# Kernel optimization log

Hardware: AMD Instinct MI355X
Metric: run time of the kernel (lower is better)

Reference implementation:

```python
import jax, jax.numpy as jnp
import numpy as np

B, L, H = 2, 2048, 2048
NH, KVH = 16, 4
D = H // NH          # 128
G = NH // KVH        # 4 query heads per kv head
LN_EPS = 1e-12


def setup_inputs() -> dict:
    key = jax.random.key(0)
    ks = jax.random.split(key, 6)
    s = 0.02
    return {
        "hidden_state": jax.random.normal(ks[0], (B, L, H), jnp.float32),
        "mask": jnp.zeros((B, 1, 1, L), jnp.float32),
        "Wq": jax.random.normal(ks[1], (H, H), jnp.float32) * s,
        "bq": jnp.zeros((H,), jnp.float32),
        "Wk": jax.random.normal(ks[2], (KVH * D, H), jnp.float32) * s,
        "bk": jnp.zeros((KVH * D,), jnp.float32),
        "Wv": jax.random.normal(ks[3], (KVH * D, H), jnp.float32) * s,
        "bv": jnp.zeros((KVH * D,), jnp.float32),
        "Wo": jax.random.normal(ks[4], (H, H), jnp.float32) * s,
        "bo": jnp.zeros((H,), jnp.float32),
        "ln_g": jnp.ones((H,), jnp.float32),
        "ln_b": jnp.zeros((H,), jnp.float32),
    }


def _layernorm(x, g, b):
    mu = jnp.mean(x, axis=-1, keepdims=True)
    var = jnp.mean(jnp.square(x - mu), axis=-1, keepdims=True)
    return (x - mu) * jax.lax.rsqrt(var + LN_EPS) * g + b


def reference(hidden_state, mask, Wq, bq, Wk, bk, Wv, bv, Wo, bo, ln_g, ln_b):
    x = hidden_state
    # projections: b l (h d)
    q = x @ Wq.T + bq            # [B,L,NH*D]
    k = x @ Wk.T + bk            # [B,L,KVH*D]
    v = x @ Wv.T + bv            # [B,L,KVH*D]
    # b l (h d) -> b h l d, with q heads grouped per kv head (GQA broadcast,
    # mathematically identical to repeat_kv + dense SDPA)
    q = q.reshape(B, L, KVH, G, D).transpose(0, 2, 3, 1, 4)   # [B,KVH,G,L,D]
    k = k.reshape(B, L, KVH, D).transpose(0, 2, 1, 3)         # [B,KVH,L,D]
    v = v.reshape(B, L, KVH, D).transpose(0, 2, 1, 3)         # [B,KVH,L,D]
    scale = 1.0 / jnp.sqrt(jnp.float32(D))
    scores = jnp.einsum('bkgld,bkmd->bkglm', q, k) * scale    # [B,KVH,G,L,L]
    scores = scores + mask[:, :, None]                         # broadcast [B,1,1,1,L]
    attn = jax.nn.softmax(scores, axis=-1)
    out = jnp.einsum('bkglm,bkmd->bkgld', attn, v)            # [B,KVH,G,L,D]
    out = out.transpose(0, 3, 1, 2, 4).reshape(B, L, H)       # b h l d -> b l (h d)
    # SelfOutput: dense + residual + layernorm
    out = out @ Wo.T + bo
    return _layernorm(out + x, ln_g, ln_b)
```

## Files before the change

### kernel.cpp

```cpp
#include <hip/hip_runtime.h>
#include <math.h>

typedef short v8s __attribute__((ext_vector_type(8)));
typedef short v4s __attribute__((ext_vector_type(4)));
typedef float v4f __attribute__((ext_vector_type(4)));
typedef unsigned long long ull;

constexpr int L_ = 2048;
constexpr int H_ = 2048;
constexpr float LOG2E = 1.4426950408889634f;
constexpr float QSCALE = 0.08838834764831845f * LOG2E;

__device__ inline unsigned short f2bf(float f) {
    unsigned int u = __float_as_uint(f);
    u += 0x7fffu + ((u >> 16) & 1u);
    return (unsigned short)(u >> 16);
}

__device__ inline unsigned int pk2bf(float lo, float hi) {
    unsigned int a = __float_as_uint(lo) + 0x8000u;
    unsigned int b = __float_as_uint(hi) + 0x8000u;
    return __builtin_amdgcn_perm(b, a, 0x07060302);
}

__device__ inline void async16(const void* g, void* l) {
    __builtin_amdgcn_global_load_lds(
        (const __attribute__((address_space(1))) unsigned int*)g,
        (__attribute__((address_space(3))) unsigned int*)l, 16, 0, 0);
}

__global__ __launch_bounds__(256) void conv_all(
    const float* __restrict__ x,  const float* __restrict__ wq,
    const float* __restrict__ wk, const float* __restrict__ wv,
    const float* __restrict__ wo, const float* __restrict__ mask,
    unsigned short* __restrict__ xb, unsigned short* __restrict__ wqkvb,
    unsigned short* __restrict__ wob, float* __restrict__ maskL)
{
    int u = blockIdx.x * 256 + threadIdx.x;
    const float* s;
    unsigned short* d;
    if (u < 1048576)      { s = x  + (size_t)u * 8;             d = xb   + (size_t)u * 8; }
    else if (u < 1572864) { size_t t = (size_t)(u - 1048576) * 8; s = wq + t; d = wqkvb + t; }
    else if (u < 1703936) { size_t t = (size_t)(u - 1572864) * 8; s = wk + t; d = wqkvb + (size_t)2048 * 2048 + t; }
    else if (u < 1835008) { size_t t = (size_t)(u - 1703936) * 8; s = wv + t; d = wqkvb + (size_t)2560 * 2048 + t; }
    else if (u < 2359296) { size_t t = (size_t)(u - 1835008) * 8; s = wo + t; d = wob + t; }
    else if (u < 2359808) {
        int m = (u - 2359296) * 8;
        float4 a = *(const float4*)(mask + m);
        float4 b = *(const float4*)(mask + m + 4);
        float4 oa = {a.x * LOG2E, a.y * LOG2E, a.z * LOG2E, a.w * LOG2E};
        float4 ob = {b.x * LOG2E, b.y * LOG2E, b.z * LOG2E, b.w * LOG2E};
        *(float4*)(maskL + m) = oa;
        *(float4*)(maskL + m + 4) = ob;
        return;
    } else return;
    float4 a = *(const float4*)s;
    float4 b = *(const float4*)(s + 4);
    v8s o;
    o[0] = (short)f2bf(a.x); o[1] = (short)f2bf(a.y);
    o[2] = (short)f2bf(a.z); o[3] = (short)f2bf(a.w);
    o[4] = (short)f2bf(b.x); o[5] = (short)f2bf(b.y);
    o[6] = (short)f2bf(b.z); o[7] = (short)f2bf(b.w);
    *(v8s*)d = o;
}

template <int MODE>
__global__ __launch_bounds__(256) void gemm_mfma(
    const unsigned short* __restrict__ A, const unsigned short* __restrict__ W,
    const float* __restrict__ b0, const float* __restrict__ b1,
    const float* __restrict__ b2,
    unsigned short* __restrict__ oq, unsigned short* __restrict__ ok,
    unsigned short* __restrict__ ov,
    float* __restrict__ of, const float* __restrict__ resid,
    int K, int N)
{
    __shared__ short SM[3 * 8192];

    const int tid  = threadIdx.x;
    const int lane = tid & 63;
    const int wave = tid >> 6;
    const int lid  = lane & 15;
    const int g    = lane >> 4;
    const int wr   = wave >> 1, wc = wave & 1;
    const int row0 = blockIdx.y * 128, col0 = blockIdx.x * 128;

    auto stage = [&](int k0, int buf) {
#pragma unroll
        for (int i = 0; i < 2; ++i) {
            int idx = tid + i * 256;
            int r = idx >> 2, s = idx & 3;
            int c = s ^ ((r >> 1) & 3);
            async16(A + (size_t)(row0 + r) * K + k0 + c * 8,
                    &SM[buf * 8192 + idx * 8]);
            async16(W + (size_t)(col0 + r) * K + k0 + c * 8,
                    &SM[buf * 8192 + 4096 + idx * 8]);
        }
    };

    v4f acc[4][4];
#pragma unroll
    for (int i = 0; i < 4; ++i)
#pragma unroll
        for (int j = 0; j < 4; ++j) acc[i][j] = (v4f){0.f, 0.f, 0.f, 0.f};

    stage(0, 0);
    stage(32, 1);
    int p = 0;
    for (int k0 = 0; k0 < K; k0 += 32) {
        __syncthreads();
        if (k0 + 64 < K) {
            int nb = p + 2; if (nb >= 3) nb -= 3;
            stage(k0 + 64, nb);
        }
        const short* As = &SM[p * 8192];
        const short* Bs = &SM[p * 8192 + 4096];

        v8s af[4], bf[4];
#pragma unroll
        for (int t = 0; t < 4; ++t) {
            int ra = wr * 64 + t * 16 + lid;
            int rb = wc * 64 + t * 16 + lid;
            af[t] = *(const v8s*)&As[ra * 32 + ((g ^ ((ra >> 1) & 3)) * 8)];
            bf[t] = *(const v8s*)&Bs[rb * 32 + ((g ^ ((rb >> 1) & 3)) * 8)];
        }
#pragma unroll
        for (int mt = 0; mt < 4; ++mt)
#pragma unroll
            for (int nt = 0; nt < 4; ++nt)
                acc[mt][nt] = __builtin_amdgcn_mfma_f32_16x16x32_bf16(
                    af[mt], bf[nt], acc[mt][nt], 0, 0, 0);
        if (++p == 3) p = 0;
    }

    const int crow = row0 + wr * 64, ccol = col0 + wc * 64;
    if (MODE == 0) {
#pragma unroll
        for (int mt = 0; mt < 4; ++mt)
#pragma unroll
            for (int nt = 0; nt < 4; ++nt) {
                int cc = ccol + nt * 16 + lid;
                float bb = b0[cc];
#pragma unroll
                for (int r = 0; r < 4; ++r) {
                    int rr = crow + mt * 16 + g * 4 + r;
                    of[(size_t)rr * N + cc] =
                        acc[mt][nt][r] + bb + resid[(size_t)rr * N + cc];
                }
            }
    } else {
        const int seg = (col0 < 2048) ? 0 : (col0 < 2560 ? 1 : 2);
#pragma unroll
        for (int mt = 0; mt < 4; ++mt)
#pragma unroll
            for (int nt = 0; nt < 4; ++nt) {
                int cc = ccol + nt * 16 + lid;
                if (seg == 0) {
                    float bb = b0[cc];
#pragma unroll
                    for (int r = 0; r < 4; ++r) {
                        int rr = crow + mt * 16 + g * 4 + r;
                        oq[(size_t)rr * 2048 + cc] =
                            f2bf((acc[mt][nt][r] + bb) * QSCALE);
                    }
                } else if (seg == 1) {
                    float bb = b1[cc - 2048];
#pragma unroll
                    for (int r = 0; r < 4; ++r) {
                        int rr = crow + mt * 16 + g * 4 + r;
                        ok[(size_t)rr * 512 + (cc - 2048)] =
                            f2bf(acc[mt][nt][r] + bb);
                    }
                } else {
                    float bb = b2[cc - 2560];
#pragma unroll
                    for (int r = 0; r < 4; ++r) {
                        int rr = crow + mt * 16 + g * 4 + r;
                        ov[(size_t)rr * 512 + (cc - 2560)] =
                            f2bf(acc[mt][nt][r] + bb);
                    }
                }
            }
    }
}

__global__ __launch_bounds__(256) void transpose_v(
    const unsigned short* __restrict__ V, unsigned short* __restrict__ Vt)
{
    __shared__ unsigned short T[64][72];
    const int r0 = blockIdx.y * 64;
    const int c0 = blockIdx.x * 64;
    const int tid = threadIdx.x;
    const int r = tid >> 3, c8 = (tid & 7) * 8;
#pragma unroll
    for (int h = 0; h < 2; ++h) {
        v8s val = *(const v8s*)&V[(size_t)(r0 + h * 32 + r) * 512 + c0 + c8];
#pragma unroll
        for (int e = 0; e < 8; ++e) T[c8 + e][h * 32 + r] = (unsigned short)val[e];
    }
    __syncthreads();
#pragma unroll
    for (int h = 0; h < 2; ++h) {
        int idx = tid + h * 256;
        int ci = idx >> 3, ch = (idx & 7) * 8;
        int t32 = ch & 32;
        int gg  = (ch >> 3) & 3;
        int kb  = t32 + gg * 4;
        uint2 lo = *(const uint2*)&T[ci][kb];
        uint2 hi = *(const uint2*)&T[ci][kb + 16];
        union { uint4 u; v8s v; } o;
        o.u.x = lo.x; o.u.y = lo.y; o.u.z = hi.x; o.u.w = hi.y;
        int rr = r0 + ch;
        *(v8s*)&Vt[((size_t)((rr >> 11) * 512 + c0 + ci)) * 2048 + (rr & 2047)] = o.v;
    }
}

__global__ __launch_bounds__(256) void flash_mfma(
    const unsigned short* __restrict__ Q,
    const unsigned short* __restrict__ K,
    const unsigned short* __restrict__ Vt,
    const float* __restrict__ maskL,
    unsigned short* __restrict__ AO)
{
    __shared__ short K_s[2][32 * 128];
    __shared__ short V_s[2][128 * 32];

    const int tid  = threadIdx.x;
    const int lane = tid & 63;
    const int wave = tid >> 6;
    const int lid  = lane & 15;
    const int g    = lane >> 4;
    const int lh   = (lid >> 2) & 3;
    const int h    = blockIdx.y;
    const int b    = blockIdx.z;
    const int kvh  = h >> 2;
    const int q0   = blockIdx.x * 128;
    const int wq   = wave * 32;

    const unsigned short* pK;
    const unsigned short* pV;
    {
        int kr = tid >> 4, ks = tid & 15;
        pK = K + ((size_t)(b * L_ + kr)) * 512 + kvh * 128 +
             ((ks ^ (kr & 15)) * 8);
        int vd = tid >> 2, vs = tid & 3;
        pV = Vt + ((size_t)(b * 512 + kvh * 128 + vd)) * 2048 +
             ((vs ^ ((vd >> 2) & 3)) * 8);
    }

    v8s bq[2][4];
    {
        const size_t base = ((size_t)(b * L_ + q0 + wq + lid)) * 2048 + h * 128;
#pragma unroll
        for (int qt = 0; qt < 2; ++qt)
#pragma unroll
            for (int kc = 0; kc < 4; ++kc)
                bq[qt][kc] = *(const v8s*)(Q + base + (size_t)qt * 16 * 2048 +
                                           kc * 32 + g * 8);
    }

    v4f oacc[2][8];
#pragma unroll
    for (int mt = 0; mt < 2; ++mt)
#pragma unroll
        for (int nt = 0; nt < 8; ++nt) oacc[mt][nt] = (v4f){0.f, 0.f, 0.f, 0.f};
    float lsm[2] = {0.f, 0.f};

    async16(pK,              &K_s[0][tid * 8]);
    async16(pK + 16 * 512,   &K_s[0][(tid + 256) * 8]);
    async16(pV,              &V_s[0][tid * 8]);
    async16(pV + 64 * 2048,  &V_s[0][(tid + 256) * 8]);

    for (int it = 0; it < 64; ++it) {
        const int p = it & 1;
        const int k0 = it * 32;
        __syncthreads();
        pK += 32 * 512;
        pV += 32;
        if (it + 1 < 64) {
            short* dK = K_s[p ^ 1];
            short* dV = V_s[p ^ 1];
            async16(pK,              &dK[tid * 8]);
            async16(pK + 16 * 512,   &dK[(tid + 256) * 8]);
            async16(pV,              &dV[tid * 8]);
            async16(pV + 64 * 2048,  &dV[(tid + 256) * 8]);
        }
        const short* Ks = K_s[p];
        const short* Vs = V_s[p];

        v4f sacc[2][2];
#pragma unroll
        for (int kt = 0; kt < 2; ++kt) {
            float4 mk = *(const float4*)&maskL[b * L_ + k0 + kt * 16 + g * 4];
            v4f seed = {mk.x, mk.y, mk.z, mk.w};
            sacc[kt][0] = seed;
            sacc[kt][1] = seed;
        }
#pragma unroll
        for (int kc = 0; kc < 4; ++kc)
#pragma unroll
            for (int kt = 0; kt < 2; ++kt) {
                v8s ak = *(const v8s*)&Ks[(kt * 16 + lid) * 128 +
                                          (((kc * 4 + g) ^ lid) * 8)];
#pragma unroll
                for (int qt = 0; qt < 2; ++qt)
                    sacc[kt][qt] = __builtin_amdgcn_mfma_f32_16x16x32_bf16(
                        ak, bq[qt][kc], sacc[kt][qt], 0, 0, 0);
            }

        v8s ap[2];
#pragma unroll
        for (int qt = 0; qt < 2; ++qt) {
            float e0 = __builtin_amdgcn_exp2f(sacc[0][qt][0]);
            float e1 = __builtin_amdgcn_exp2f(sacc[0][qt][1]);
            float e2 = __builtin_amdgcn_exp2f(sacc[0][qt][2]);
            float e3 = __builtin_amdgcn_exp2f(sacc[0][qt][3]);
            float f0 = __builtin_amdgcn_exp2f(sacc[1][qt][0]);
            float f1 = __builtin_amdgcn_exp2f(sacc[1][qt][1]);
            float f2 = __builtin_amdgcn_exp2f(sacc[1][qt][2]);
            float f3 = __builtin_amdgcn_exp2f(sacc[1][qt][3]);
            lsm[qt] += ((e0 + e1) + (e2 + e3)) + ((f0 + f1) + (f2 + f3));
            union { uint4 u; v8s v; } pa;
            pa.u.x = pk2bf(e0, e1);
            pa.u.y = pk2bf(e2, e3);
            pa.u.z = pk2bf(f0, f1);
            pa.u.w = pk2bf(f2, f3);
            ap[qt] = pa.v;
        }

#pragma unroll
        for (int nt = 0; nt < 8; ++nt) {
            v8s bv = *(const v8s*)&Vs[(nt * 16 + lid) * 32 + ((g ^ lh) * 8)];
#pragma unroll
            for (int mt = 0; mt < 2; ++mt)
                oacc[mt][nt] = __builtin_amdgcn_mfma_f32_16x16x32_bf16(
                    ap[mt], bv, oacc[mt][nt], 0, 0, 0);
        }
    }

#pragma unroll
    for (int qt = 0; qt < 2; ++qt) {
        lsm[qt] += __shfl_xor(lsm[qt], 16);
        lsm[qt] += __shfl_xor(lsm[qt], 32);
    }
#pragma unroll
    for (int mt = 0; mt < 2; ++mt) {
        float linv[4];
#pragma unroll
        for (int r = 0; r < 4; ++r) linv[r] = 1.0f / __shfl(lsm[mt], g * 4 + r);
#pragma unroll
        for (int nt = 0; nt < 8; ++nt)
#pragma unroll
            for (int r = 0; r < 4; ++r) {
                size_t orow = (size_t)(b * L_ + q0 + wq + mt * 16 + g * 4 + r);
                AO[orow * 2048 + h * 128 + nt * 16 + lid] =
                    f2bf(oacc[mt][nt][r] * linv[r]);
            }
    }
}

__global__ __launch_bounds__(256) void ln_kernel(
    const float* __restrict__ P, const float* __restrict__ g,
    const float* __restrict__ bta, float* __restrict__ Out)
{
    const int row = blockIdx.x;
    const int tid = threadIdx.x;
    const float* p = P + (size_t)row * H_;

    float vals[8];
    float s = 0.f;
#pragma unroll
    for (int it = 0; it < 2; ++it) {
        int c = tid * 4 + it * 1024;
        float4 a = *(const float4*)&p[c];
        vals[it * 4 + 0] = a.x; vals[it * 4 + 1] = a.y;
        vals[it * 4 + 2] = a.z; vals[it * 4 + 3] = a.w;
        s += a.x + a.y + a.z + a.w;
    }
    __shared__ float red[4];
    float t = s;
#pragma unroll
    for (int off = 32; off > 0; off >>= 1) t += __shfl_xor(t, off);
    if ((tid & 63) == 0) red[tid >> 6] = t;
    __syncthreads();
    float mean = (red[0] + red[1] + red[2] + red[3]) * (1.f / (float)H_);

    float vsum = 0.f;
#pragma unroll
    for (int i = 0; i < 8; ++i) {
        float d = vals[i] - mean;
        vsum += d * d;
    }
    __syncthreads();
    t = vsum;
#pragma unroll
    for (int off = 32; off > 0; off >>= 1) t += __shfl_xor(t, off);
    if ((tid & 63) == 0) red[tid >> 6] = t;
    __syncthreads();
    float var = (red[0] + red[1] + red[2] + red[3]) * (1.f / (float)H_);
    float rs  = 1.f / sqrtf(var + 1e-12f);

#pragma unroll
    for (int it = 0; it < 2; ++it) {
        int c = tid * 4 + it * 1024;
        float4 gv = *(const float4*)&g[c];
        float4 bv = *(const float4*)&bta[c];
        float4 ov;
        ov.x = (vals[it * 4 + 0] - mean) * rs * gv.x + bv.x;
        ov.y = (vals[it * 4 + 1] - mean) * rs * gv.y + bv.y;
        ov.z = (vals[it * 4 + 2] - mean) * rs * gv.z + bv.z;
        ov.w = (vals[it * 4 + 3] - mean) * rs * gv.w + bv.w;
        *(float4*)&Out[(size_t)row * H_ + c] = ov;
    }
}

extern "C" void kernel_launch(void* const* d_in, const int* in_sizes, int n_in,
                              void* d_out, int out_size, void* d_ws, size_t ws_size,
                              hipStream_t stream)
{
    const float* x    = (const float*)d_in[0];
    const float* mask = (const float*)d_in[1];
    const float* Wq   = (const float*)d_in[2];
    const float* bq   = (const float*)d_in[3];
    const float* Wk   = (const float*)d_in[4];
    const float* bk   = (const float*)d_in[5];
    const float* Wv   = (const float*)d_in[6];
    const float* bv   = (const float*)d_in[7];
    const float* Wo   = (const float*)d_in[8];
    const float* bo   = (const float*)d_in[9];
    const float* lng  = (const float*)d_in[10];
    const float* lnb  = (const float*)d_in[11];
    float* out = (float*)d_out;

    char* ws = (char*)d_ws;
    unsigned short* xb    = (unsigned short*)(ws);
    unsigned short* wqkv  = (unsigned short*)(ws + 16777216);
    float*          maskL = (float*)         (ws + 29360128);
    unsigned short* q     = (unsigned short*)(ws + 29376512);
    unsigned short* k     = (unsigned short*)(ws + 46153728);
    unsigned short* vnat  = (unsigned short*)(ws + 50348032);
    unsigned short* vt    = (unsigned short*)(ws + 54542336);
    unsigned short* ao    = (unsigned short*)(ws + 58736640);
    unsigned short* wob   = (unsigned short*)(ws + 75513856);
    float*          pj    = (float*)(ws);

    dim3 blk(256);
    conv_all<<<9218, blk, 0, stream>>>(x, Wq, Wk, Wv, Wo, mask,
                                       xb, wqkv, wob, maskL);

    gemm_mfma<3><<<dim3(24, 32), blk, 0, stream>>>(
        xb, wqkv, bq, bk, bv, q, k, vnat, nullptr, nullptr, 2048, 3072);

    transpose_v<<<dim3(8, 64), blk, 0, stream>>>(vnat, vt);

    flash_mfma<<<dim3(16, 16, 2), dim3(256), 0, stream>>>(q, k, vt, maskL, ao);

    gemm_mfma<0><<<dim3(16, 32), blk, 0, stream>>>(
        ao, wob, bo, nullptr, nullptr, nullptr, nullptr, nullptr, pj, x, 2048, 2048);
    ln_kernel<<<4096, blk, 0, stream>>>(pj, lng, lnb, out);
}
```

Before: 353.4 us.

## Triple-buffer K/V tiles with explicit vmcnt waits and stage mask in LDS

Turns the flash-attention K/V pipeline from double to triple buffering, prefetching two tiles ahead. Each iteration now uses an explicit s_waitcnt vmcnt plus a raw s_barrier in place of __syncthreads, so loads stay in flight across iterations. The additive mask row is also copied once into shared memory instead of being read from global memory every tile. This grows LDS use per block (extra K/V buffers plus 8KB of mask), which may lower occupancy. The hand-counted vmcnt assumes the async copies are the only outstanding vector loads.

```diff
diff --git a/kernel.cpp b/kernel.cpp
--- a/kernel.cpp
+++ b/kernel.cpp
@@ -221,8 +221,9 @@
     const float* __restrict__ maskL,
     unsigned short* __restrict__ AO)
 {
-    __shared__ short K_s[2][32 * 128];
-    __shared__ short V_s[2][128 * 32];
+    __shared__ short K_s[3][32 * 128];
+    __shared__ short V_s[3][128 * 32];
+    __shared__ float maskS[2048];
 
     const int tid  = threadIdx.x;
     const int lane = tid & 63;
@@ -236,6 +237,14 @@
     const int q0   = blockIdx.x * 128;
     const int wq   = wave * 32;
 
+    {
+        float4 m0 = *(const float4*)&maskL[b * L_ + tid * 8];
+        float4 m1 = *(const float4*)&maskL[b * L_ + tid * 8 + 4];
+        *(float4*)&maskS[tid * 8]     = m0;
+        *(float4*)&maskS[tid * 8 + 4] = m1;
+        asm volatile("s_waitcnt lgkmcnt(0)" ::: "memory");
+    }
+
     const unsigned short* pK;
     const unsigned short* pV;
     {
@@ -247,6 +256,15 @@
              ((vs ^ ((vd >> 2) & 3)) * 8);
     }
 
+    auto stage = [&](const unsigned short* sK, const unsigned short* sV, int buf) {
+        short* dK = K_s[buf];
+        short* dV = V_s[buf];
+        async16(sK,             &dK[tid * 8]);
+        async16(sK + 16 * 512,  &dK[(tid + 256) * 8]);
+        async16(sV,             &dV[tid * 8]);
+        async16(sV + 64 * 2048, &dV[(tid + 256) * 8]);
+    };
+
     v8s bq[2][4];
     {
         const size_t base = ((size_t)(b * L_ + q0 + wq + lid)) * 2048 + h * 128;
@@ -265,32 +283,33 @@
         for (int nt = 0; nt < 8; ++nt) oacc[mt][nt] = (v4f){0.f, 0.f, 0.f, 0.f};
     float lsm[2] = {0.f, 0.f};
 
-    async16(pK,              &K_s[0][tid * 8]);
-    async16(pK + 16 * 512,   &K_s[0][(tid + 256) * 8]);
-    async16(pV,              &V_s[0][tid * 8]);
-    async16(pV + 64 * 2048,  &V_s[0][(tid + 256) * 8]);
-
+    stage(pK, pV, 0);
+    stage(pK + 32 * 512, pV + 32, 1);
+    pK += 64 * 512;
+    pV += 64;
+
+    int p = 0;
     for (int it = 0; it < 64; ++it) {
-        const int p = it & 1;
-        const int k0 = it * 32;
-        __syncthreads();
-        pK += 32 * 512;
-        pV += 32;
-        if (it + 1 < 64) {
-            short* dK = K_s[p ^ 1];
-            short* dV = V_s[p ^ 1];
-            async16(pK,              &dK[tid * 8]);
-            async16(pK + 16 * 512,   &dK[(tid + 256) * 8]);
-            async16(pV,              &dV[tid * 8]);
-            async16(pV + 64 * 2048,  &dV[(tid + 256) * 8]);
-        }
+        if (it < 63) asm volatile("s_waitcnt vmcnt(4)" ::: "memory");
+        else         asm volatile("s_waitcnt vmcnt(0)" ::: "memory");
+        __builtin_amdgcn_s_barrier();
+        __builtin_amdgcn_sched_barrier(0);
+
+        if (it + 2 < 64) {
+            int nb = p + 2; if (nb >= 3) nb -= 3;
+            stage(pK, pV, nb);
+            pK += 32 * 512;
+            pV += 32;
+        }
+
         const short* Ks = K_s[p];
         const short* Vs = V_s[p];
+        const int k0 = it * 32;
 
         v4f sacc[2][2];
 #pragma unroll
         for (int kt = 0; kt < 2; ++kt) {
-            float4 mk = *(const float4*)&maskL[b * L_ + k0 + kt * 16 + g * 4];
+            float4 mk = *(const float4*)&maskS[k0 + kt * 16 + g * 4];
             v4f seed = {mk.x, mk.y, mk.z, mk.w};
             sacc[kt][0] = seed;
             sacc[kt][1] = seed;
@@ -335,6 +354,8 @@
                 oacc[mt][nt] = __builtin_amdgcn_mfma_f32_16x16x32_bf16(
                     ap[mt], bv, oacc[mt][nt], 0, 0, 0);
         }
+
+        if (++p == 3) p = 0;
     }
 
 #pragma unroll
```

Measured after the change: 354.3 us. About the same (+0.3%).

## Load K/V tiles directly into registers in flash attention, drop LDS staging

Applied to the files above, without the earlier changes.

Flash attention stops staging K and V tiles through double-buffered shared memory with barriers. Each wave now loads its MFMA operands straight from global memory into registers, prefetching the next tile after each MFMA phase, and wraps the MFMA phases in s_setprio. The grid becomes 1D with remapped block indices so blocks sharing a KV head and batch run close together for cache reuse, and launch bounds request 2 blocks per SIMD. This removes LDS traffic and syncthreads, but each wave re-fetches K/V from L2 and register pressure rises.

```diff
diff --git a/kernel.cpp b/kernel.cpp
--- a/kernel.cpp
+++ b/kernel.cpp
@@ -214,38 +214,31 @@
     }
 }
 
-__global__ __launch_bounds__(256) void flash_mfma(
+__global__ __launch_bounds__(256, 2) void flash_mfma(
     const unsigned short* __restrict__ Q,
     const unsigned short* __restrict__ K,
     const unsigned short* __restrict__ Vt,
     const float* __restrict__ maskL,
     unsigned short* __restrict__ AO)
 {
-    __shared__ short K_s[2][32 * 128];
-    __shared__ short V_s[2][128 * 32];
-
     const int tid  = threadIdx.x;
     const int lane = tid & 63;
     const int wave = tid >> 6;
     const int lid  = lane & 15;
     const int g    = lane >> 4;
-    const int lh   = (lid >> 2) & 3;
-    const int h    = blockIdx.y;
-    const int b    = blockIdx.z;
-    const int kvh  = h >> 2;
-    const int q0   = blockIdx.x * 128;
-    const int wq   = wave * 32;
-
-    const unsigned short* pK;
-    const unsigned short* pV;
-    {
-        int kr = tid >> 4, ks = tid & 15;
-        pK = K + ((size_t)(b * L_ + kr)) * 512 + kvh * 128 +
-             ((ks ^ (kr & 15)) * 8);
-        int vd = tid >> 2, vs = tid & 3;
-        pV = Vt + ((size_t)(b * 512 + kvh * 128 + vd)) * 2048 +
-             ((vs ^ ((vd >> 2) & 3)) * 8);
-    }
+
+    const int bid = blockIdx.x;
+    const int xm  = bid & 7;
+    const int r_  = bid >> 3;
+    const int h   = xm * 2 + (r_ & 1);
+    const int b   = (r_ >> 1) & 1;
+    const int q0  = (r_ >> 2) * 128;
+    const int kvh = h >> 2;
+    const int wq  = wave * 32;
+
+    const unsigned short* Kb = K  + ((size_t)b * L_) * 512 + kvh * 128;
+    const unsigned short* Vb = Vt + ((size_t)(b * 512 + kvh * 128)) * 2048;
+    const float*          mb = maskL + b * L_;
 
     v8s bq[2][4];
     {
@@ -265,47 +258,49 @@
         for (int nt = 0; nt < 8; ++nt) oacc[mt][nt] = (v4f){0.f, 0.f, 0.f, 0.f};
     float lsm[2] = {0.f, 0.f};
 
-    async16(pK,              &K_s[0][tid * 8]);
-    async16(pK + 16 * 512,   &K_s[0][(tid + 256) * 8]);
-    async16(pV,              &V_s[0][tid * 8]);
-    async16(pV + 64 * 2048,  &V_s[0][(tid + 256) * 8]);
+    v8s ak[2][4], vv[8];
+#pragma unroll
+    for (int kt = 0; kt < 2; ++kt)
+#pragma unroll
+        for (int kc = 0; kc < 4; ++kc)
+            ak[kt][kc] = *(const v8s*)(Kb + (size_t)(kt * 16 + lid) * 512 +
+                                       kc * 32 + g * 8);
+#pragma unroll
+    for (int nt = 0; nt < 8; ++nt)
+        vv[nt] = *(const v8s*)(Vb + (size_t)(nt * 16 + lid) * 2048 + g * 8);
 
     for (int it = 0; it < 64; ++it) {
-        const int p = it & 1;
         const int k0 = it * 32;
-        __syncthreads();
-        pK += 32 * 512;
-        pV += 32;
-        if (it + 1 < 64) {
-            short* dK = K_s[p ^ 1];
-            short* dV = V_s[p ^ 1];
-            async16(pK,              &dK[tid * 8]);
-            async16(pK + 16 * 512,   &dK[(tid + 256) * 8]);
-            async16(pV,              &dV[tid * 8]);
-            async16(pV + 64 * 2048,  &dV[(tid + 256) * 8]);
-        }
-        const short* Ks = K_s[p];
-        const short* Vs = V_s[p];
 
         v4f sacc[2][2];
 #pragma unroll
         for (int kt = 0; kt < 2; ++kt) {
-            float4 mk = *(const float4*)&maskL[b * L_ + k0 + kt * 16 + g * 4];
+            float4 mk = *(const float4*)&mb[k0 + kt * 16 + g * 4];
             v4f seed = {mk.x, mk.y, mk.z, mk.w};
             sacc[kt][0] = seed;
             sacc[kt][1] = seed;
         }
+        __builtin_amdgcn_s_setprio(1);
 #pragma unroll
         for (int kc = 0; kc < 4; ++kc)
 #pragma unroll
-            for (int kt = 0; kt < 2; ++kt) {
-                v8s ak = *(const v8s*)&Ks[(kt * 16 + lid) * 128 +
-                                          (((kc * 4 + g) ^ lid) * 8)];
+            for (int kt = 0; kt < 2; ++kt)
 #pragma unroll
                 for (int qt = 0; qt < 2; ++qt)
                     sacc[kt][qt] = __builtin_amdgcn_mfma_f32_16x16x32_bf16(
-                        ak, bq[qt][kc], sacc[kt][qt], 0, 0, 0);
-            }
+                        ak[kt][kc], bq[qt][kc], sacc[kt][qt], 0, 0, 0);
+        __builtin_amdgcn_s_setprio(0);
+
+        __builtin_amdgcn_sched_barrier(0);
+        if (it < 63) {
+            const int kn = k0 + 32 + lid;
+#pragma unroll
+            for (int kt = 0; kt < 2; ++kt)
+#pragma unroll
+                for (int kc = 0; kc < 4; ++kc)
+                    ak[kt][kc] = *(const v8s*)(Kb +
+                        (size_t)(kn + kt * 16) * 512 + kc * 32 + g * 8);
+        }
 
         v8s ap[2];
 #pragma unroll
@@ -327,13 +322,21 @@
             ap[qt] = pa.v;
         }
 
-#pragma unroll
-        for (int nt = 0; nt < 8; ++nt) {
-            v8s bv = *(const v8s*)&Vs[(nt * 16 + lid) * 32 + ((g ^ lh) * 8)];
+        __builtin_amdgcn_s_setprio(1);
+#pragma unroll
+        for (int nt = 0; nt < 8; ++nt)
 #pragma unroll
             for (int mt = 0; mt < 2; ++mt)
                 oacc[mt][nt] = __builtin_amdgcn_mfma_f32_16x16x32_bf16(
-                    ap[mt], bv, oacc[mt][nt], 0, 0, 0);
+                    ap[mt], vv[nt], oacc[mt][nt], 0, 0, 0);
+        __builtin_amdgcn_s_setprio(0);
+
+        __builtin_amdgcn_sched_barrier(0);
+        if (it < 63) {
+            const int cn = k0 + 32 + g * 8;
+#pragma unroll
+            for (int nt = 0; nt < 8; ++nt)
+                vv[nt] = *(const v8s*)(Vb + (size_t)(nt * 16 + lid) * 2048 + cn);
         }
     }
 
@@ -452,7 +455,7 @@
 
     transpose_v<<<dim3(8, 64), blk, 0, stream>>>(vnat, vt);
 
-    flash_mfma<<<dim3(16, 16, 2), dim3(256), 0, stream>>>(q, k, vt, maskL, ao);
+    flash_mfma<<<dim3(512), dim3(256), 0, stream>>>(q, k, vt, maskL, ao);
 
     gemm_mfma<0><<<dim3(16, 32), blk, 0, stream>>>(
         ao, wob, bo, nullptr, nullptr, nullptr, nullptr, nullptr, pj, x, 2048, 2048);
```

Result: slower. 484.6 us (+37.1%).

## Fuse V transpose into QKV GEMM epilogue and enlarge flash blocks

Applied to the files above, without the earlier changes.

The QKV GEMM epilogue now writes V directly in the transposed, permuted layout the flash kernel expects, so the separate transpose_v kernel and its round trip through global memory go away. The flash kernel moves to 512-thread blocks covering 256 query rows, so each K/V tile staged in shared memory is reused by twice as many queries. Blocks are indexed on a 1D grid that puts blocks sharing a KV head and batch next to each other, to improve L2 reuse. The risks are scattered 8-byte epilogue stores and lower occupancy or register pressure from the larger blocks.

```diff
diff --git a/kernel.cpp b/kernel.cpp
--- a/kernel.cpp
+++ b/kernel.cpp
@@ -172,49 +172,24 @@
                     }
                 } else {
                     float bb = b2[cc - 2560];
-#pragma unroll
-                    for (int r = 0; r < 4; ++r) {
-                        int rr = crow + mt * 16 + g * 4 + r;
-                        ov[(size_t)rr * 512 + (cc - 2560)] =
-                            f2bf(acc[mt][nt][r] + bb);
-                    }
+                    int dprime = cc - 2560;
+                    int colb = (crow & 2047) + ((mt >> 1) << 5) +
+                               (g << 3) + ((mt & 1) << 2);
+                    size_t vrow = (size_t)((crow >> 11) * 512 + dprime);
+                    unsigned int lo =
+                        (unsigned int)f2bf(acc[mt][nt][0] + bb) |
+                        ((unsigned int)f2bf(acc[mt][nt][1] + bb) << 16);
+                    unsigned int hi =
+                        (unsigned int)f2bf(acc[mt][nt][2] + bb) |
+                        ((unsigned int)f2bf(acc[mt][nt][3] + bb) << 16);
+                    uint2 pkv; pkv.x = lo; pkv.y = hi;
+                    *(uint2*)&ov[vrow * 2048 + colb] = pkv;
                 }
             }
     }
 }
 
-__global__ __launch_bounds__(256) void transpose_v(
-    const unsigned short* __restrict__ V, unsigned short* __restrict__ Vt)
-{
-    __shared__ unsigned short T[64][72];
-    const int r0 = blockIdx.y * 64;
-    const int c0 = blockIdx.x * 64;
-    const int tid = threadIdx.x;
-    const int r = tid >> 3, c8 = (tid & 7) * 8;
-#pragma unroll
-    for (int h = 0; h < 2; ++h) {
-        v8s val = *(const v8s*)&V[(size_t)(r0 + h * 32 + r) * 512 + c0 + c8];
-#pragma unroll
-        for (int e = 0; e < 8; ++e) T[c8 + e][h * 32 + r] = (unsigned short)val[e];
-    }
-    __syncthreads();
-#pragma unroll
-    for (int h = 0; h < 2; ++h) {
-        int idx = tid + h * 256;
-        int ci = idx >> 3, ch = (idx & 7) * 8;
-        int t32 = ch & 32;
-        int gg  = (ch >> 3) & 3;
-        int kb  = t32 + gg * 4;
-        uint2 lo = *(const uint2*)&T[ci][kb];
-        uint2 hi = *(const uint2*)&T[ci][kb + 16];
-        union { uint4 u; v8s v; } o;
-        o.u.x = lo.x; o.u.y = lo.y; o.u.z = hi.x; o.u.w = hi.y;
-        int rr = r0 + ch;
-        *(v8s*)&Vt[((size_t)((rr >> 11) * 512 + c0 + ci)) * 2048 + (rr & 2047)] = o.v;
-    }
-}
-
-__global__ __launch_bounds__(256) void flash_mfma(
+__global__ __launch_bounds__(512) void flash_mfma(
     const unsigned short* __restrict__ Q,
     const unsigned short* __restrict__ K,
     const unsigned short* __restrict__ Vt,
@@ -230,10 +205,13 @@
     const int lid  = lane & 15;
     const int g    = lane >> 4;
     const int lh   = (lid >> 2) & 3;
-    const int h    = blockIdx.y;
-    const int b    = blockIdx.z;
-    const int kvh  = h >> 2;
-    const int q0   = blockIdx.x * 128;
+
+    const int c7   = blockIdx.x & 7;
+    const int kvh  = c7 >> 1;
+    const int b    = c7 & 1;
+    const int rest = blockIdx.x >> 3;
+    const int h    = kvh * 4 + (rest & 3);
+    const int q0   = (rest >> 2) * 256;
     const int wq   = wave * 32;
 
     const unsigned short* pK;
@@ -265,10 +243,8 @@
         for (int nt = 0; nt < 8; ++nt) oacc[mt][nt] = (v4f){0.f, 0.f, 0.f, 0.f};
     float lsm[2] = {0.f, 0.f};
 
-    async16(pK,              &K_s[0][tid * 8]);
-    async16(pK + 16 * 512,   &K_s[0][(tid + 256) * 8]);
-    async16(pV,              &V_s[0][tid * 8]);
-    async16(pV + 64 * 2048,  &V_s[0][(tid + 256) * 8]);
+    async16(pK, &K_s[0][tid * 8]);
+    async16(pV, &V_s[0][tid * 8]);
 
     for (int it = 0; it < 64; ++it) {
         const int p = it & 1;
@@ -277,12 +253,8 @@
         pK += 32 * 512;
         pV += 32;
         if (it + 1 < 64) {
-            short* dK = K_s[p ^ 1];
-            short* dV = V_s[p ^ 1];
-            async16(pK,              &dK[tid * 8]);
-            async16(pK + 16 * 512,   &dK[(tid + 256) * 8]);
-            async16(pV,              &dV[tid * 8]);
-            async16(pV + 64 * 2048,  &dV[(tid + 256) * 8]);
+            async16(pK, &K_s[p ^ 1][tid * 8]);
+            async16(pV, &V_s[p ^ 1][tid * 8]);
         }
         const short* Ks = K_s[p];
         const short* Vs = V_s[p];
@@ -437,7 +409,6 @@
     float*          maskL = (float*)         (ws + 29360128);
     unsigned short* q     = (unsigned short*)(ws + 29376512);
     unsigned short* k     = (unsigned short*)(ws + 46153728);
-    unsigned short* vnat  = (unsigned short*)(ws + 50348032);
     unsigned short* vt    = (unsigned short*)(ws + 54542336);
     unsigned short* ao    = (unsigned short*)(ws + 58736640);
     unsigned short* wob   = (unsigned short*)(ws + 75513856);
@@ -448,11 +419,9 @@
                                        xb, wqkv, wob, maskL);
 
     gemm_mfma<3><<<dim3(24, 32), blk, 0, stream>>>(
-        xb, wqkv, bq, bk, bv, q, k, vnat, nullptr, nullptr, 2048, 3072);
-
-    transpose_v<<<dim3(8, 64), blk, 0, stream>>>(vnat, vt);
-
-    flash_mfma<<<dim3(16, 16, 2), dim3(256), 0, stream>>>(q, k, vt, maskL, ao);
+        xb, wqkv, bq, bk, bv, q, k, vt, nullptr, nullptr, 2048, 3072);
+
+    flash_mfma<<<dim3(256), dim3(512), 0, stream>>>(q, k, vt, maskL, ao);
 
     gemm_mfma<0><<<dim3(16, 32), blk, 0, stream>>>(
         ao, wob, bo, nullptr, nullptr, nullptr, nullptr, nullptr, pj, x, 2048, 2048);
```

New measurement: 343.0 us. 1.03x faster.
